# Kernel tuning notes

Measured on AMD Instinct MI355X. Metric: run time of the kernel, lower is better.

The kernel has to match this reference:

```python
import jax, jax.numpy as jnp
import numpy as np

N_NODES = 100000
N_EDGES = 1600000
D_IN = 128
D_OUT = 128


def setup_inputs() -> dict:
    key = jax.random.key(0)
    k_x, k_w, k_r, k_c, k_v = jax.random.split(key, 5)
    x = jax.random.normal(k_x, (N_NODES, D_IN), dtype=jnp.float32)
    # xavier_uniform: U(-a, a), a = sqrt(6/(fan_in+fan_out))
    a = float(np.sqrt(6.0 / (D_IN + D_OUT)))
    W = jax.random.uniform(k_w, (D_IN, D_OUT), dtype=jnp.float32, minval=-a, maxval=a)
    edge_row = jax.random.randint(k_r, (N_EDGES,), 0, N_NODES, dtype=jnp.int32)
    edge_col = jax.random.randint(k_c, (N_EDGES,), 0, N_NODES, dtype=jnp.int32)
    edge_val = jax.random.uniform(k_v, (N_EDGES,), dtype=jnp.float32)
    return {"x": x, "W": W, "edge_row": edge_row, "edge_col": edge_col, "edge_val": edge_val}


def reference(x, W, edge_row, edge_col, edge_val):
    # dropout with p=0.0 is the identity (module default), so omitted.
    support = x @ W                                  # [N, D_OUT] dense GEMM
    # sparse adj @ support in COO form: out[r] += v * support[c]
    msgs = support[edge_col] * edge_val[:, None]      # [E, D_OUT] irregular gather
    out = jax.ops.segment_sum(msgs, edge_row, num_segments=x.shape[0])
    return jnp.tanh(out)
```

## Files before the change

### kernel.cpp

```cpp
#include <hip/hip_runtime.h>
#include <hip/hip_bf16.h>
#include <hip/hip_fp16.h>
#include <math.h>

#define D 128
#define BIN_SHIFT 9
#define BIN_ROWS 512
#define NB_MAX 256
#define CPAD 16
#define AW 8192

typedef _Float16 half8 __attribute__((ext_vector_type(8)));
typedef float floatx4 __attribute__((ext_vector_type(4)));

__global__ void gcn_wt_kernel(const float* __restrict__ W,
                              unsigned short* __restrict__ wt,
                              int* __restrict__ cbin) {
    const int i = blockIdx.x * 256 + threadIdx.x;
    const int n = i >> 7, k = i & 127;
    wt[i] = __half_as_ushort(__float2half_rn(W[k * D + n]));
    if (blockIdx.x == 0) cbin[threadIdx.x] = 0;
}

__global__ __launch_bounds__(256) void gcn_gemm_kernel(
        const float* __restrict__ x, const unsigned short* __restrict__ wt,
        unsigned short* __restrict__ support2, int n_nodes) {
    const int wave = threadIdx.x >> 6;
    const int lane = threadIdx.x & 63;
    const int q = lane >> 4;
    const int n16 = lane & 15;
    const int row_base = blockIdx.x * 128 + wave * 32;
    if (row_base >= n_nodes) return;

    const half8* wt8 = (const half8*)wt;

    floatx4 acc[2][8];
#pragma unroll
    for (int mt = 0; mt < 2; ++mt)
#pragma unroll
        for (int nt = 0; nt < 8; ++nt) acc[mt][nt] = (floatx4){0.f, 0.f, 0.f, 0.f};

#pragma unroll
    for (int kc = 0; kc < 4; ++kc) {
        half8 b[8];
#pragma unroll
        for (int nt = 0; nt < 8; ++nt)
            b[nt] = wt8[(nt * 16 + n16) * 16 + kc * 4 + q];
#pragma unroll
        for (int mt = 0; mt < 2; ++mt) {
            const float* xp = x + (size_t)(row_base + mt * 16 + n16) * D
                                + kc * 32 + q * 8;
            const float4 f0 = *(const float4*)xp;
            const float4 f1 = *(const float4*)(xp + 4);
            half8 a;
            a[0] = (_Float16)f0.x; a[1] = (_Float16)f0.y;
            a[2] = (_Float16)f0.z; a[3] = (_Float16)f0.w;
            a[4] = (_Float16)f1.x; a[5] = (_Float16)f1.y;
            a[6] = (_Float16)f1.z; a[7] = (_Float16)f1.w;
#pragma unroll
            for (int nt = 0; nt < 8; ++nt)
                acc[mt][nt] = __builtin_amdgcn_mfma_f32_16x16x32_f16(
                    a, b[nt], acc[mt][nt], 0, 0, 0);
        }
    }

#pragma unroll
    for (int mt = 0; mt < 2; ++mt) {
        const int r0 = row_base + mt * 16 + q * 4;
#pragma unroll
        for (int nt = 0; nt < 8; ++nt) {
            const int col = nt * 16 + n16;
#pragma unroll
            for (int i = 0; i < 4; ++i)
                support2[(size_t)(r0 + i) * D + col] =
                    __half_as_ushort(__float2half_rn(acc[mt][nt][i]));
        }
    }
}

__global__ __launch_bounds__(256) void gcn_chist_kernel(
        const int* __restrict__ erow, int* __restrict__ cbin, int n_edges) {
    __shared__ int h[NB_MAX];
    const int t = threadIdx.x;
    h[t] = 0;
    __syncthreads();
    const int stride = gridDim.x * 256 * 4;
    const int nv = n_edges & ~3;
    for (int i = (blockIdx.x * 256 + t) * 4; i + 3 < n_edges; i += stride) {
        const int4 r = *(const int4*)(erow + i);
        atomicAdd(&h[r.x >> BIN_SHIFT], 1);
        atomicAdd(&h[r.y >> BIN_SHIFT], 1);
        atomicAdd(&h[r.z >> BIN_SHIFT], 1);
        atomicAdd(&h[r.w >> BIN_SHIFT], 1);
    }
    if (blockIdx.x == 0) {
        for (int i = nv + t; i < n_edges; i += 256)
            atomicAdd(&h[erow[i] >> BIN_SHIFT], 1);
    }
    __syncthreads();
    if (h[t] > 0) atomicAdd(&cbin[t], h[t]);
}

__global__ void gcn_cscan_kernel(const int* __restrict__ cbin,
                                 int* __restrict__ cbase,
                                 int* __restrict__ ccur,
                                 int* __restrict__ offsets,
                                 int nbins, int n_nodes, int n_edges) {
    __shared__ int sm[256];
    const int t = threadIdx.x;
    const int v = (t < nbins) ? cbin[t] : 0;
    sm[t] = v;
    __syncthreads();
    for (int off = 1; off < 256; off <<= 1) {
        int tv = (t >= off) ? sm[t - off] : 0;
        __syncthreads();
        sm[t] += tv;
        __syncthreads();
    }
    const int ex = sm[t] - v;
    if (t < nbins) { cbase[t] = ex; ccur[t * CPAD] = ex; }
    if (t == 0) { cbase[nbins] = n_edges; offsets[n_nodes] = n_edges; }
}

__global__ __launch_bounds__(256) void gcn_binA_kernel(
        const int* __restrict__ erow, const int* __restrict__ ecol,
        const float* __restrict__ eval, int* __restrict__ ccur,
        uint2* __restrict__ tmp8, int n_edges, int nbins) {
    __shared__ uint2 recs[AW];
    __shared__ int hist[NB_MAX];
    __shared__ int lstart[NB_MAX];
    __shared__ int gbase[NB_MAX];
    const int t = threadIdx.x;
    const int w0 = blockIdx.x * AW;
    const int wend = min(w0 + AW, n_edges);
    const int cnt = wend - w0;

    for (int i = t; i < NB_MAX; i += 256) hist[i] = 0;
    __syncthreads();

    for (int i = w0 + t; i < wend; i += 256)
        atomicAdd(&hist[erow[i] >> BIN_SHIFT], 1);
    __syncthreads();

    {
        const int v = hist[t];
        gbase[t] = v;
        __syncthreads();
        for (int off = 1; off < 256; off <<= 1) {
            int tv = (t >= off) ? gbase[t - off] : 0;
            __syncthreads();
            gbase[t] += tv;
            __syncthreads();
        }
        lstart[t] = gbase[t] - v;
        __syncthreads();
    }

    {
        const int c = hist[t];
        int gb = 0;
        if (t < nbins && c > 0) gb = atomicAdd(&ccur[t * CPAD], c);
        __syncthreads();
        gbase[t] = gb;
        hist[t] = lstart[t];
    }
    __syncthreads();

    for (int i = w0 + t; i < wend; i += 256) {
        const int r = erow[i];
        const int c = ecol[i];
        const unsigned short vh = __half_as_ushort(__float2half_rn(eval[i]));
        const int b = r >> BIN_SHIFT;
        const int p = atomicAdd(&hist[b], 1);
        recs[p] = make_uint2(((unsigned)r << 15) | vh, (unsigned)c);
    }
    __syncthreads();

    for (int s = t; s < cnt; s += 256) {
        const uint2 rec = recs[s];
        const int b = (int)(rec.x >> 15) >> BIN_SHIFT;
        tmp8[gbase[b] + (s - lstart[b])] = rec;
    }
}

__global__ __launch_bounds__(256) void gcn_binB_kernel(
        const uint2* __restrict__ tmp8, const int* __restrict__ cbase,
        int* __restrict__ offsets,
        unsigned int* __restrict__ rec4, int n_nodes) {
    __shared__ int cnt[BIN_ROWS];
    __shared__ int sm[256];
    const int bin = blockIdx.x;
    const int r0 = bin << BIN_SHIFT;
    const int t = threadIdx.x;
    cnt[t] = 0;
    cnt[t + 256] = 0;
    __syncthreads();

    const int beg = cbase[bin];
    const int end = cbase[bin + 1];

    for (int i = beg + t; i < end; i += 256) {
        const int r = (int)(tmp8[i].x >> 15);
        atomicAdd(&cnt[r - r0], 1);
    }
    __syncthreads();

    const int c0 = cnt[2 * t], c1 = cnt[2 * t + 1];
    const int s = c0 + c1;
    sm[t] = s;
    __syncthreads();
    for (int off = 1; off < 256; off <<= 1) {
        int tv = (t >= off) ? sm[t - off] : 0;
        __syncthreads();
        sm[t] += tv;
        __syncthreads();
    }
    const int pbase = beg + sm[t] - s;

    cnt[2 * t] = pbase;
    cnt[2 * t + 1] = pbase + c0;
    const int row0 = r0 + 2 * t;
    if (row0 < n_nodes) offsets[row0] = pbase;
    if (row0 + 1 < n_nodes) offsets[row0 + 1] = pbase + c0;
    __syncthreads();

    for (int i = beg + t; i < end; i += 256) {
        const uint2 p = tmp8[i];
        const int r = (int)(p.x >> 15);
        const int pos = atomicAdd(&cnt[r - r0], 1);
        rec4[pos] = (p.y << 15) | (p.x & 0x7FFFu);
    }
}

__global__ __launch_bounds__(256) void gcn_gather_kernel(
        const unsigned int* __restrict__ support_u,
        const unsigned int* __restrict__ rec4,
        const int* __restrict__ offsets,
        float* __restrict__ out, int n_nodes) {
    const int node = __builtin_amdgcn_readfirstlane(
        blockIdx.x * 4 + (threadIdx.x >> 6));
    const int lane = threadIdx.x & 63;
    if (node >= n_nodes) return;

    const int beg = offsets[node];
    const int end = offsets[node + 1];

    float ax = 0.f, ay = 0.f, bx = 0.f, by = 0.f;
    int e = beg;
    for (; e + 3 < end; e += 4) {
        const unsigned r0 = rec4[e + 0];
        const unsigned r1 = rec4[e + 1];
        const unsigned r2 = rec4[e + 2];
        const unsigned r3 = rec4[e + 3];
        const unsigned s0 = support_u[(size_t)(r0 >> 15) * 64 + lane];
        const unsigned s1 = support_u[(size_t)(r1 >> 15) * 64 + lane];
        const unsigned s2 = support_u[(size_t)(r2 >> 15) * 64 + lane];
        const unsigned s3 = support_u[(size_t)(r3 >> 15) * 64 + lane];
        const float v0 = __half2float(__ushort_as_half((unsigned short)(r0 & 0x7FFFu)));
        const float v1 = __half2float(__ushort_as_half((unsigned short)(r1 & 0x7FFFu)));
        const float v2 = __half2float(__ushort_as_half((unsigned short)(r2 & 0x7FFFu)));
        const float v3 = __half2float(__ushort_as_half((unsigned short)(r3 & 0x7FFFu)));
        ax += v0 * __half2float(__ushort_as_half((unsigned short)(s0 & 0xFFFFu)));
        ay += v0 * __half2float(__ushort_as_half((unsigned short)(s0 >> 16)));
        bx += v1 * __half2float(__ushort_as_half((unsigned short)(s1 & 0xFFFFu)));
        by += v1 * __half2float(__ushort_as_half((unsigned short)(s1 >> 16)));
        ax += v2 * __half2float(__ushort_as_half((unsigned short)(s2 & 0xFFFFu)));
        ay += v2 * __half2float(__ushort_as_half((unsigned short)(s2 >> 16)));
        bx += v3 * __half2float(__ushort_as_half((unsigned short)(s3 & 0xFFFFu)));
        by += v3 * __half2float(__ushort_as_half((unsigned short)(s3 >> 16)));
    }
    for (; e < end; ++e) {
        const unsigned r = rec4[e];
        const unsigned s = support_u[(size_t)(r >> 15) * 64 + lane];
        const float v = __half2float(__ushort_as_half((unsigned short)(r & 0x7FFFu)));
        ax += v * __half2float(__ushort_as_half((unsigned short)(s & 0xFFFFu)));
        ay += v * __half2float(__ushort_as_half((unsigned short)(s >> 16)));
    }

    float2* out2 = (float2*)out;
    out2[(size_t)node * 64 + lane] = make_float2(tanhf(ax + bx), tanhf(ay + by));
}

extern "C" void kernel_launch(void* const* d_in, const int* in_sizes, int n_in,
                              void* d_out, int out_size, void* d_ws, size_t ws_size,
                              hipStream_t stream) {
    const float* x    = (const float*)d_in[0];
    const float* W    = (const float*)d_in[1];
    const int*   erow = (const int*)d_in[2];
    const int*   ecol = (const int*)d_in[3];
    const float* eval = (const float*)d_in[4];
    float* out = (float*)d_out;

    const int n_nodes = in_sizes[0] / D;
    const int n_edges = in_sizes[2];
    const int nbins = (n_nodes + BIN_ROWS - 1) >> BIN_SHIFT;

    unsigned short* support2 = (unsigned short*)d_ws;
    unsigned short* wt = support2 + (size_t)n_nodes * D;
    uint2* tmp8   = (uint2*)(wt + D * D);
    unsigned int* rec4 = (unsigned int*)(tmp8 + n_edges);
    int*  offsets = (int*)(rec4 + n_edges);
    int*  cbin    = offsets + n_nodes + 1;
    int*  cbase   = cbin + NB_MAX;
    int*  ccur    = cbase + NB_MAX + 1;

    gcn_wt_kernel<<<(D * D) / 256, 256, 0, stream>>>(W, wt, cbin);
    gcn_gemm_kernel<<<(n_nodes + 127) / 128, 256, 0, stream>>>(
        x, wt, support2, n_nodes);

    gcn_chist_kernel<<<320, 256, 0, stream>>>(erow, cbin, n_edges);
    gcn_cscan_kernel<<<1, 256, 0, stream>>>(cbin, cbase, ccur, offsets,
                                            nbins, n_nodes, n_edges);

    gcn_binA_kernel<<<(n_edges + AW - 1) / AW, 256, 0, stream>>>(
        erow, ecol, eval, ccur, tmp8, n_edges, nbins);
    gcn_binB_kernel<<<nbins, 256, 0, stream>>>(tmp8, cbase, offsets, rec4, n_nodes);

    gcn_gather_kernel<<<(n_nodes + 3) / 4, 256, 0, stream>>>(
        (const unsigned int*)support2, rec4, offsets, out, n_nodes);
}
```

Measured before the change: 259.7 us.

## Sub-sort edges by column bucket within rows, unroll gather by eight, nontemporal stores

The per-bin counting sort now keys each edge by row plus a 16-way column bucket (col >> 13), so the edges inside each row come out grouped by source-column range. It uses a transposed shared-memory layout for the 8192 counters and a per-thread serial scan over 32 slots. The aim is better locality of the support gathers across nearby rows. The gather loop also issues eight independent row loads per iteration to expose more memory-level parallelism, and the output is written with nontemporal stores to avoid cache pollution. In exchange the binning kernel uses more shared memory and does more scan work.

```diff
diff --git a/kernel.cpp b/kernel.cpp
--- a/kernel.cpp
+++ b/kernel.cpp
@@ -9,9 +9,15 @@
 #define NB_MAX 256
 #define CPAD 16
 #define AW 8192
+#define NCB 16
+#define CB_SHIFT 13
+#define CKEYS (BIN_ROWS * NCB)
 
 typedef _Float16 half8 __attribute__((ext_vector_type(8)));
 typedef float floatx4 __attribute__((ext_vector_type(4)));
+typedef float floatx2 __attribute__((ext_vector_type(2)));
+
+__device__ __forceinline__ int cslot(int k) { return ((k & 31) << 8) | (k >> 5); }
 
 __global__ void gcn_wt_kernel(const float* __restrict__ W,
                               unsigned short* __restrict__ wt,
@@ -187,27 +193,28 @@
         const uint2* __restrict__ tmp8, const int* __restrict__ cbase,
         int* __restrict__ offsets,
         unsigned int* __restrict__ rec4, int n_nodes) {
-    __shared__ int cnt[BIN_ROWS];
+    __shared__ int cnt[CKEYS];
     __shared__ int sm[256];
     const int bin = blockIdx.x;
     const int r0 = bin << BIN_SHIFT;
     const int t = threadIdx.x;
-    cnt[t] = 0;
-    cnt[t + 256] = 0;
+    for (int i = t; i < CKEYS; i += 256) cnt[i] = 0;
     __syncthreads();
 
     const int beg = cbase[bin];
     const int end = cbase[bin + 1];
 
     for (int i = beg + t; i < end; i += 256) {
-        const int r = (int)(tmp8[i].x >> 15);
-        atomicAdd(&cnt[r - r0], 1);
-    }
-    __syncthreads();
-
-    const int c0 = cnt[2 * t], c1 = cnt[2 * t + 1];
-    const int s = c0 + c1;
-    sm[t] = s;
+        const uint2 p = tmp8[i];
+        const int k = (((int)(p.x >> 15) - r0) << 4) | (int)(p.y >> CB_SHIFT);
+        atomicAdd(&cnt[cslot(k)], 1);
+    }
+    __syncthreads();
+
+    int sum = 0;
+#pragma unroll
+    for (int i = 0; i < 32; ++i) sum += cnt[(i << 8) | t];
+    sm[t] = sum;
     __syncthreads();
     for (int off = 1; off < 256; off <<= 1) {
         int tv = (t >= off) ? sm[t - off] : 0;
@@ -215,19 +222,26 @@
         sm[t] += tv;
         __syncthreads();
     }
-    const int pbase = beg + sm[t] - s;
-
-    cnt[2 * t] = pbase;
-    cnt[2 * t + 1] = pbase + c0;
-    const int row0 = r0 + 2 * t;
-    if (row0 < n_nodes) offsets[row0] = pbase;
-    if (row0 + 1 < n_nodes) offsets[row0 + 1] = pbase + c0;
+    int run = sm[t] - sum;
+#pragma unroll
+    for (int i = 0; i < 32; ++i) {
+        const int s = (i << 8) | t;
+        const int c = cnt[s];
+        cnt[s] = run;
+        run += c;
+    }
+    __syncthreads();
+
+    for (int lr = t; lr < BIN_ROWS; lr += 256) {
+        const int row = r0 + lr;
+        if (row < n_nodes) offsets[row] = beg + cnt[cslot(lr << 4)];
+    }
     __syncthreads();
 
     for (int i = beg + t; i < end; i += 256) {
         const uint2 p = tmp8[i];
-        const int r = (int)(p.x >> 15);
-        const int pos = atomicAdd(&cnt[r - r0], 1);
+        const int k = (((int)(p.x >> 15) - r0) << 4) | (int)(p.y >> CB_SHIFT);
+        const int pos = beg + atomicAdd(&cnt[cslot(k)], 1);
         rec4[pos] = (p.y << 15) | (p.x & 0x7FFFu);
     }
 }
@@ -247,27 +261,37 @@
 
     float ax = 0.f, ay = 0.f, bx = 0.f, by = 0.f;
     int e = beg;
+    for (; e + 7 < end; e += 8) {
+        unsigned r[8], s[8];
+#pragma unroll
+        for (int j = 0; j < 8; ++j) r[j] = rec4[e + j];
+#pragma unroll
+        for (int j = 0; j < 8; ++j)
+            s[j] = support_u[(size_t)(r[j] >> 15) * 64 + lane];
+#pragma unroll
+        for (int j = 0; j < 8; ++j) {
+            const float v = __half2float(__ushort_as_half((unsigned short)(r[j] & 0x7FFFu)));
+            const float slo = __half2float(__ushort_as_half((unsigned short)(s[j] & 0xFFFFu)));
+            const float shi = __half2float(__ushort_as_half((unsigned short)(s[j] >> 16)));
+            if (j & 1) { bx += v * slo; by += v * shi; }
+            else       { ax += v * slo; ay += v * shi; }
+        }
+    }
     for (; e + 3 < end; e += 4) {
-        const unsigned r0 = rec4[e + 0];
-        const unsigned r1 = rec4[e + 1];
-        const unsigned r2 = rec4[e + 2];
-        const unsigned r3 = rec4[e + 3];
-        const unsigned s0 = support_u[(size_t)(r0 >> 15) * 64 + lane];
-        const unsigned s1 = support_u[(size_t)(r1 >> 15) * 64 + lane];
-        const unsigned s2 = support_u[(size_t)(r2 >> 15) * 64 + lane];
-        const unsigned s3 = support_u[(size_t)(r3 >> 15) * 64 + lane];
-        const float v0 = __half2float(__ushort_as_half((unsigned short)(r0 & 0x7FFFu)));
-        const float v1 = __half2float(__ushort_as_half((unsigned short)(r1 & 0x7FFFu)));
-        const float v2 = __half2float(__ushort_as_half((unsigned short)(r2 & 0x7FFFu)));
-        const float v3 = __half2float(__ushort_as_half((unsigned short)(r3 & 0x7FFFu)));
-        ax += v0 * __half2float(__ushort_as_half((unsigned short)(s0 & 0xFFFFu)));
-        ay += v0 * __half2float(__ushort_as_half((unsigned short)(s0 >> 16)));
-        bx += v1 * __half2float(__ushort_as_half((unsigned short)(s1 & 0xFFFFu)));
-        by += v1 * __half2float(__ushort_as_half((unsigned short)(s1 >> 16)));
-        ax += v2 * __half2float(__ushort_as_half((unsigned short)(s2 & 0xFFFFu)));
-        ay += v2 * __half2float(__ushort_as_half((unsigned short)(s2 >> 16)));
-        bx += v3 * __half2float(__ushort_as_half((unsigned short)(s3 & 0xFFFFu)));
-        by += v3 * __half2float(__ushort_as_half((unsigned short)(s3 >> 16)));
+        unsigned r[4], s[4];
+#pragma unroll
+        for (int j = 0; j < 4; ++j) r[j] = rec4[e + j];
+#pragma unroll
+        for (int j = 0; j < 4; ++j)
+            s[j] = support_u[(size_t)(r[j] >> 15) * 64 + lane];
+#pragma unroll
+        for (int j = 0; j < 4; ++j) {
+            const float v = __half2float(__ushort_as_half((unsigned short)(r[j] & 0x7FFFu)));
+            const float slo = __half2float(__ushort_as_half((unsigned short)(s[j] & 0xFFFFu)));
+            const float shi = __half2float(__ushort_as_half((unsigned short)(s[j] >> 16)));
+            if (j & 1) { bx += v * slo; by += v * shi; }
+            else       { ax += v * slo; ay += v * shi; }
+        }
     }
     for (; e < end; ++e) {
         const unsigned r = rec4[e];
@@ -277,8 +301,11 @@
         ay += v * __half2float(__ushort_as_half((unsigned short)(s >> 16)));
     }
 
-    float2* out2 = (float2*)out;
-    out2[(size_t)node * 64 + lane] = make_float2(tanhf(ax + bx), tanhf(ay + by));
+    floatx2 res;
+    res.x = tanhf(ax + bx);
+    res.y = tanhf(ay + by);
+    floatx2* out2 = (floatx2*)out;
+    __builtin_nontemporal_store(res, &out2[(size_t)node * 64 + lane]);
 }
 
 extern "C" void kernel_launch(void* const* d_in, const int* in_sizes, int n_in,
```

Result: no change. 260.9 us (+0.5%).
